# Performance work log

Measured on AMD Instinct MI355X. Metric: run time of the kernel, lower is better.

The kernel has to match this reference:

```python
import jax, jax.numpy as jnp
import numpy as np

B, C, N, T = 8, 32, 4000, 12
KT = 3
TS = 6          # tem_size
SUP_ORD_CH = (2 * 3 + 1) * C  # (order*support_len+1)*c_in = 224
EPS = 1e-5


def setup_inputs() -> dict:
    key = jax.random.key(0)
    ks = jax.random.split(key, 20)
    inp = {
        "x": jax.random.normal(ks[0], (B, C, N, T), dtype=jnp.float32),
        # dense normalized supports (scaled uniform, like row-normalized adjacency)
        "A0": jax.random.uniform(ks[1], (N, N), dtype=jnp.float32) / N,
        "A1": jax.random.uniform(ks[2], (N, N), dtype=jnp.float32) / N,
        "A2": jax.random.uniform(ks[3], (N, N), dtype=jnp.float32) / N,
        # conv1: 1x1 Conv2d(32 -> 32), bias
        "conv1_w": jax.random.normal(ks[4], (C, C), dtype=jnp.float32) * 0.05,
        "conv1_b": jnp.zeros((C,), dtype=jnp.float32),
        # multigcn mlp: Conv2d(224 -> 64, kernel (1, Kt)), bias
        "mlp_w": jax.random.normal(ks[5], (2 * C, SUP_ORD_CH, 1, KT), dtype=jnp.float32) * 0.02,
        "mlp_b": jnp.zeros((2 * C,), dtype=jnp.float32),
        # conv_temp1: 1x1 Conv2d over time axis (10 -> 6), bias
        "ct1_w": jax.random.normal(ks[6], (TS, T - KT + 1), dtype=jnp.float32) * 0.1,
        "ct1_b": jnp.zeros((TS,), dtype=jnp.float32),
        # TATT_1 params
        "tat_c1_w": jax.random.normal(ks[7], (C,), dtype=jnp.float32) * 0.1,   # Conv2d(c_in->1,1x1,no bias)
        "tat_c2_w": jax.random.normal(ks[8], (N,), dtype=jnp.float32) * 0.01,  # Conv2d(N->1,1x1,no bias)
        "tat_w": jax.random.normal(ks[9], (N, C), dtype=jnp.float32) * 0.01,
        "tat_bias": jnp.zeros((TS, TS), dtype=jnp.float32),
        "tat_v": jax.random.normal(ks[10], (TS, TS), dtype=jnp.float32) * 0.3,
        "bn1_g": jnp.ones((TS,), dtype=jnp.float32),
        "bn1_b": jnp.zeros((TS,), dtype=jnp.float32),
        # final BatchNorm2d(c_out)
        "bn2_g": jnp.ones((C,), dtype=jnp.float32),
        "bn2_b": jnp.zeros((C,), dtype=jnp.float32),
    }
    return inp


def reference(x, A0, A1, A2, conv1_w, conv1_b, mlp_w, mlp_b, ct1_w, ct1_b,
              tat_c1_w, tat_c2_w, tat_w, tat_bias, tat_v, bn1_g, bn1_b,
              bn2_g, bn2_b):
    # residual = conv1(x)  (1x1 conv over channels)
    residual = jnp.einsum('oc,bcnl->bonl', conv1_w, x) + conv1_b[None, :, None, None]

    # multi_gcn_time: nconv does A<-A.T then einsum('ncvl,vw->ncwl'),
    # i.e. out[..,w,..] = sum_v x[..,v,..] * A[w,v]
    outs = [x]
    for A in (A0, A1, A2):
        x1 = jnp.einsum('bcvl,wv->bcwl', x, A)
        outs.append(x1)
        x2 = jnp.einsum('bcvl,wv->bcwl', x1, A)
        outs.append(x2)
    h = jnp.concatenate(outs, axis=1)  # (B, 224, N, T)
    h = jax.lax.conv_general_dilated(
        h, mlp_w, window_strides=(1, 1), padding='VALID',
        dimension_numbers=('NCHW', 'OIHW', 'NCHW')) + mlp_b[None, :, None, None]  # (B,64,N,10)

    # gated tanh * sigmoid
    x1, x2 = jnp.split(h, 2, axis=1)
    g = jnp.tanh(x1) * jax.nn.sigmoid(x2)  # (B,32,N,10)

    # conv_temp1: 1x1 conv over the TIME axis (10 -> 6)
    g = jnp.einsum('ql,bcnl->bcnq', ct1_w, g) + ct1_b[None, None, None, :]  # (B,32,N,6)

    # TATT_1 temporal attention coefficients
    f1 = jnp.einsum('c,bcnt->btn', tat_c1_w, g)                       # (B,6,N)
    f2 = jnp.einsum('n,bcnt->bct', tat_c2_w, g)                       # (B,32,6)
    logits = jax.nn.sigmoid(jnp.einsum('btn,nc,bcs->bts', f1, tat_w, f2) + tat_bias)
    logits = jnp.einsum('ts,bsq->btq', tat_v, logits)                 # (B,6,6)
    # BatchNorm1d(tem_size) applied after permute(0,2,1): channel = q axis
    lp = jnp.transpose(logits, (0, 2, 1))
    mu = lp.mean(axis=(0, 2), keepdims=True)
    var = lp.var(axis=(0, 2), keepdims=True)
    lp = (lp - mu) / jnp.sqrt(var + EPS) * bn1_g[None, :, None] + bn1_b[None, :, None]
    logits = jnp.transpose(lp, (0, 2, 1))
    coefs = jax.nn.softmax(logits, axis=-1)                           # (B,6,6)

    # x = einsum('bcnl,blq->bcnq', x, T_coef.transpose(-1,-2))
    Tc = jnp.transpose(coefs, (0, 2, 1))
    out = jnp.einsum('bcnl,blq->bcnq', g, Tc)                         # (B,32,N,6)

    y = out + residual[:, :, :, -out.shape[3]:]
    # BatchNorm2d(c_out), training-mode batch stats
    mu2 = y.mean(axis=(0, 2, 3), keepdims=True)
    var2 = y.var(axis=(0, 2, 3), keepdims=True)
    return (y - mu2) / jnp.sqrt(var2 + EPS) * bn2_g[None, :, None, None] + bn2_b[None, :, None, None]
```

## Files before the change

kernel.cpp:

```cpp
#include <hip/hip_runtime.h>
#include <hip/hip_bf16.h>
#include <cstdint>
#include <cstddef>


typedef __attribute__((ext_vector_type(8))) short s16x8;
typedef __attribute__((ext_vector_type(4))) short s16x4;
typedef __attribute__((ext_vector_type(4))) float f32x4;

#define DEVFN __device__ __forceinline__

DEVFN void gload16(const void* g, void* l) {
  __builtin_amdgcn_global_load_lds((const __attribute__((address_space(1))) unsigned int*)g,
                                   (__attribute__((address_space(3))) unsigned int*)l, 16, 0, 0);
}

DEVFN unsigned short f2bf(float f) {
  union { float f; unsigned int u; } v; v.f = f;
  unsigned int u = v.u;
  return (unsigned short)((u + 0x7fffu + ((u >> 16) & 1u)) >> 16);
}

__global__ void k_transpose(const float* __restrict__ x,
                            unsigned short* __restrict__ Xt,
                            unsigned short* __restrict__ Scat) {
  __shared__ float ldsT[32 * 417];
  int v0 = blockIdx.x * 32;
  int b = blockIdx.y;
  int tid = threadIdx.x;
  for (int i = tid; i < 1024; i += 256) {
    int c = i >> 5, vv = i & 31;
    const float* src = x + ((size_t)(b * 32 + c) * 4000 + v0 + vv) * 12;
    f32x4 a0 = *(const f32x4*)(src);
    f32x4 a1 = *(const f32x4*)(src + 4);
    f32x4 a2 = *(const f32x4*)(src + 8);
    float* d = ldsT + c * 417 + vv * 13;
    d[0] = a0.x; d[1] = a0.y; d[2] = a0.z; d[3] = a0.w;
    d[4] = a1.x; d[5] = a1.y; d[6] = a1.z; d[7] = a1.w;
    d[8] = a2.x; d[9] = a2.y; d[10] = a2.z; d[11] = a2.w;
  }
  __syncthreads();
  for (int unit = tid; unit < 384; unit += 256) {
    int l = unit >> 5, c = unit & 31;
    alignas(16) unsigned short tmp[32];
#pragma unroll
    for (int vv = 0; vv < 32; ++vv) tmp[vv] = f2bf(ldsT[c * 417 + vv * 13 + l]);
    unsigned short* dst = Xt + (size_t)(b * 384 + l * 32 + c) * 4096 + v0;
#pragma unroll
    for (int j = 0; j < 4; ++j) *(s16x8*)(dst + j * 8) = *(const s16x8*)(tmp + j * 8);
  }
  for (int unit = tid; unit < 384; unit += 256) {
    int l = unit >> 5, vv = unit & 31;
    alignas(16) unsigned short tmp[32];
#pragma unroll
    for (int c = 0; c < 32; ++c) tmp[c] = f2bf(ldsT[c * 417 + vv * 13 + l]);
    unsigned short* dst = Scat + ((size_t)(b * 4000 + v0 + vv) * 12 + l) * 224;
#pragma unroll
    for (int j = 0; j < 4; ++j) *(s16x8*)(dst + j * 8) = *(const s16x8*)(tmp + j * 8);
  }
}

__global__ void k_castA(const float* __restrict__ A, unsigned short* __restrict__ Abf) {
  int idx = blockIdx.x * 256 + threadIdx.x;
  int r = idx >> 10;
  int c4 = (idx & 1023) << 2;
  alignas(8) unsigned short o[4] = {0, 0, 0, 0};
  if (r < 4000 && c4 < 4000) {
    f32x4 v = *(const f32x4*)(A + (size_t)r * 4000 + c4);
    o[0] = f2bf(v.x); o[1] = f2bf(v.y); o[2] = f2bf(v.z); o[3] = f2bf(v.w);
  }
  *(s16x4*)(Abf + (size_t)r * 4096 + c4) = *(const s16x4*)o;
}

__global__ void k_wcat(const float* __restrict__ mlp_w, unsigned short* __restrict__ Wcat) {
  int i = blockIdx.x * 256 + threadIdx.x;
  if (i >= 64 * 672) return;
  int oc = i / 672, k = i % 672;
  int kt = k / 224, ic = k % 224;
  Wcat[i] = f2bf(mlp_w[((size_t)oc * 224 + ic) * 3 + kt]);
}

#define MFMA_(a, b, c) __builtin_amdgcn_mfma_f32_16x16x32_bf16(a, b, c, 0, 0, 0)

#define STGA(d, t) do {                                                          \
    const unsigned short* _s = aSrc + (size_t)(t) * 64;                          \
    unsigned short* _l = smem + (d) * 12288;                                     \
    gload16(_s,          _l + tid * 8);                                          \
    gload16(_s + 262144, _l + (512 + tid) * 8);                                  \
    gload16(_s + 524288, _l + (1024 + tid) * 8);                                 \
  } while (0)

#define STGB(d, h, t) do {                                                       \
    const unsigned short* _s = bSrc + (size_t)(h) * 524288 + (size_t)(t) * 64;   \
    unsigned short* _l = smem + 24576 + ((d) * 2 + (h)) * 8192;                  \
    gload16(_s,          _l + tid * 8);                                          \
    gload16(_s + 262144, _l + (512 + tid) * 8);                                  \
  } while (0)

#define LDA_(d, f, kk) (*(const s16x8*)(smem + (d) * 12288 + aoff + (f) * 1024 + ((kk) ? sxor : 0)))
#define LDB_(d, nf, kk) (*(const s16x8*)(smem + 24576 + ((d) * 2 + hb) * 8192 + boff + (nf) * 1024 + ((kk) ? sxor : 0)))

#define PHASE(d, mp, FIRST, STAGE_CODE, VM) do {                                 \
    s16x8 a00 = LDA_(d, 2 * (mp), 0),     a01 = LDA_(d, 2 * (mp), 1);            \
    s16x8 a10 = LDA_(d, 2 * (mp) + 1, 0), a11 = LDA_(d, 2 * (mp) + 1, 1);        \
    if (FIRST) {                                                                 \
      _Pragma("unroll")                                                          \
      for (int nf = 0; nf < 4; ++nf) { bfr[nf][0] = LDB_(d, nf, 0); bfr[nf][1] = LDB_(d, nf, 1); } \
    }                                                                            \
    STAGE_CODE;                                                                  \
    if (VM) asm volatile("s_waitcnt vmcnt(2)" ::: "memory");                     \
    __builtin_amdgcn_s_barrier();                                                \
    asm volatile("s_waitcnt lgkmcnt(0)" ::: "memory");                           \
    __builtin_amdgcn_s_setprio(1);                                               \
    _Pragma("unroll")                                                            \
    for (int nf = 0; nf < 4; ++nf) {                                             \
      acc[2 * (mp)][nf]     = MFMA_(a00, bfr[nf][0], acc[2 * (mp)][nf]);         \
      acc[2 * (mp)][nf]     = MFMA_(a01, bfr[nf][1], acc[2 * (mp)][nf]);         \
      acc[2 * (mp) + 1][nf] = MFMA_(a10, bfr[nf][0], acc[2 * (mp) + 1][nf]);     \
      acc[2 * (mp) + 1][nf] = MFMA_(a11, bfr[nf][1], acc[2 * (mp) + 1][nf]);     \
    }                                                                            \
    __builtin_amdgcn_s_setprio(0);                                               \
  } while (0)

template <int WRITE_C1>
__global__ __launch_bounds__(512, 2)
void k_gemm(const unsigned short* __restrict__ P, const unsigned short* __restrict__ Q,
            unsigned short* __restrict__ C1, unsigned short* __restrict__ Scat, int jcol) {
  extern __shared__ unsigned short smem[];
  int tid = threadIdx.x;
  int w = tid >> 6, lane = tid & 63;
  int lr = lane & 15, g = lane >> 4;
  int mq = w >> 2, nq = w & 3;
  int bid = blockIdx.x;
  int xcd = bid & 7, lid = bid >> 3;
  int nt = xcd * 2 + (lid >> 4);
  int mt = lid & 15;
  int m0 = mt * 192, n0 = nt * 256;
  int hb = nq >> 1;
  int slot0 = (g ^ (lr & 7)) * 8;
  int sxor = (slot0 & 32) ? -32 : 32;
  int aoff = (mq * 96 + lr) * 64 + slot0;
  int boff = ((nq & 1) * 64 + lr) * 64 + slot0;
  int gk = ((tid & 7) ^ ((tid >> 3) & 7)) * 8;
  const unsigned short* aSrc = P + (size_t)(m0 + (tid >> 3)) * 4096 + gk;
  const unsigned short* bSrc = Q + (size_t)(n0 + (tid >> 3)) * 4096 + gk;
  f32x4 acc[6][4] = {};
  s16x8 bfr[4][2];

  STGA(0, 0);
  STGB(0, 0, 0); STGB(0, 1, 0);
  STGB(1, 0, 1);
  asm volatile("s_waitcnt vmcnt(2)" ::: "memory");
  __builtin_amdgcn_s_barrier();

#pragma unroll 1
  for (int i = 0; i < 32; ++i) {
    int t1 = 2 * i + 1, t2 = 2 * i + 2, t3 = 2 * i + 3;
    PHASE(0, 0, 1, STGB(1, 1, t1), 0);
    PHASE(0, 1, 0, STGA(1, t1),    0);
    PHASE(0, 2, 0, STGB(0, 0, t2), 1);
    PHASE(1, 0, 1, STGB(0, 1, t2), 0);
    PHASE(1, 1, 0, STGA(0, t2),    0);
    PHASE(1, 2, 0, STGB(1, 0, t3), 1);
  }

  asm volatile("s_waitcnt vmcnt(0) lgkmcnt(0)" ::: "memory");
  __syncthreads();
  unsigned short* eld = smem;
  int rb = g * 4;
#pragma unroll
  for (int f = 0; f < 6; ++f)
#pragma unroll
    for (int nf = 0; nf < 4; ++nf)
#pragma unroll
      for (int r = 0; r < 4; ++r)
        eld[(mq * 96 + f * 16 + rb + r) * 264 + nq * 64 + nf * 16 + lr] = f2bf(acc[f][nf][r]);
  __syncthreads();
  if (WRITE_C1) {
#pragma unroll
    for (int uu = 0; uu < 2; ++uu) {
      int u = uu * 512 + tid;
      if (u < 768) {
        int row = u >> 2, q = u & 3;
        unsigned short* dst = C1 + (size_t)(m0 + row) * 4096 + n0 + q * 64;
        const unsigned short* sp = eld + row * 264 + q * 64;
#pragma unroll
        for (int j = 0; j < 8; ++j) *(s16x8*)(dst + j * 8) = *(const s16x8*)(sp + j * 8);
      }
    }
  }
  int bb2 = m0 / 384, lb = (m0 % 384) >> 5;
#pragma unroll
  for (int uu = 0; uu < 3; ++uu) {
    int u = uu * 512 + tid;
    int lg = u >> 8, nl = u & 255;
    int node = n0 + nl;
    if (node < 4000) {
      alignas(16) unsigned short tmp[32];
#pragma unroll
      for (int c = 0; c < 32; ++c) tmp[c] = eld[(lg * 32 + c) * 264 + nl];
      unsigned short* d2 = Scat + ((size_t)(bb2 * 4000 + node) * 12 + lb + lg) * 224 + jcol;
#pragma unroll
      for (int j = 0; j < 4; ++j) *(s16x8*)(d2 + j * 8) = *(const s16x8*)(tmp + j * 8);
    }
  }
}

__global__ __launch_bounds__(256, 2)
void k_mlp(const unsigned short* __restrict__ Wcat, const unsigned short* __restrict__ Scat,
           const float* __restrict__ mlp_b, float* __restrict__ G) {
  __shared__ unsigned short lds[2048 + 8192];
  unsigned short* Ws = lds;
  unsigned short* Bs = lds + 2048;
  int tid = threadIdx.x;
  int bn0 = blockIdx.x * 256;
  int t = blockIdx.y;
  int w = tid >> 6, lane = tid & 63;
  int lr = lane & 15, lk = (lane >> 4) * 8;
  f32x4 acc[4][4] = {};
  const unsigned short* gw = Wcat + (size_t)(tid >> 2) * 672 + (tid & 3) * 8;
  const unsigned short* gq = Scat + ((size_t)(bn0 + (tid >> 2)) * 12 + t) * 224 + (tid & 3) * 8;
  unsigned short* lw = Ws + tid * 8;
  unsigned short* lq = Bs + tid * 8;
  for (int s = 0; s < 21; ++s) {
    gload16(gw + s * 32, lw);
#pragma unroll
    for (int r = 0; r < 4; ++r)
      gload16(gq + (size_t)r * 64 * 2688 + s * 32, lq + r * 2048);
    __syncthreads();
    s16x8 a[4], bb[4];
#pragma unroll
    for (int f = 0; f < 4; ++f) {
      a[f] = *(const s16x8*)(Ws + (f * 16 + lr) * 32 + lk);
      bb[f] = *(const s16x8*)(Bs + (w * 64 + f * 16 + lr) * 32 + lk);
    }
#pragma unroll
    for (int fm = 0; fm < 4; ++fm)
#pragma unroll
      for (int fn = 0; fn < 4; ++fn)
        acc[fm][fn] = __builtin_amdgcn_mfma_f32_16x16x32_bf16(a[fm], bb[fn], acc[fm][fn], 0, 0, 0);
    __syncthreads();
  }
  int rbase = (lane >> 4) * 4;
#pragma unroll
  for (int fn = 0; fn < 4; ++fn) {
    int bn = bn0 + w * 64 + fn * 16 + lr;
    int b = bn / 4000;
    int n = bn - b * 4000;
    float* gbase = G + (size_t)(b * 10 + t) * 32 * 4096 + n;
#pragma unroll
    for (int fm = 0; fm < 2; ++fm)
#pragma unroll
      for (int r = 0; r < 4; ++r) {
        int c = fm * 16 + rbase + r;
        float v1 = acc[fm][fn][r] + mlp_b[c];
        float v2 = acc[fm + 2][fn][r] + mlp_b[c + 32];
        gbase[(size_t)c * 4096] = tanhf(v1) * (1.0f / (1.0f + __expf(-v2)));
      }
  }
}

__global__ void k_ct1(const float* __restrict__ G, const float* __restrict__ ct1_w,
                      const float* __restrict__ ct1_b, float* __restrict__ g6) {
  int idx = blockIdx.x * 256 + threadIdx.x;
  if (idx >= 8 * 32 * 4000) return;
  int n = idx % 4000;
  int c = (idx / 4000) % 32;
  int b = idx / (4000 * 32);
  const float* gp = G + ((size_t)(b * 10) * 32 + c) * 4096 + n;
  float v[10];
#pragma unroll
  for (int l = 0; l < 10; ++l) v[l] = gp[(size_t)l * 32 * 4096];
  float* o = g6 + (size_t)idx * 6;
#pragma unroll
  for (int q = 0; q < 6; ++q) {
    float a = ct1_b[q];
#pragma unroll
    for (int l = 0; l < 10; ++l) a += ct1_w[q * 10 + l] * v[l];
    o[q] = a;
  }
}

__global__ void k_f1(const float* __restrict__ g6, const float* __restrict__ c1,
                     float* __restrict__ f1) {
  int idx = blockIdx.x * 128 + threadIdx.x;
  if (idx >= 8 * 4000) return;
  int n = idx % 4000, b = idx / 4000;
  float acc[6] = {};
  const float* gp = g6 + ((size_t)b * 32 * 4000 + n) * 6;
  for (int c = 0; c < 32; ++c) {
    float wv = c1[c];
    const float* p = gp + (size_t)c * 4000 * 6;
#pragma unroll
    for (int t = 0; t < 6; ++t) acc[t] += wv * p[t];
  }
  for (int t = 0; t < 6; ++t) f1[((size_t)b * 6 + t) * 4000 + n] = acc[t];
}

__global__ void k_f2(const float* __restrict__ g6, const float* __restrict__ c2,
                     float* __restrict__ f2) {
  __shared__ float red[256 * 6];
  int bc = blockIdx.x;
  int tid = threadIdx.x;
  float acc[6] = {};
  const float* gp = g6 + (size_t)bc * 4000 * 6;
  for (int n = tid; n < 4000; n += 256) {
    float wv = c2[n];
#pragma unroll
    for (int t = 0; t < 6; ++t) acc[t] += wv * gp[(size_t)n * 6 + t];
  }
  for (int t = 0; t < 6; ++t) red[tid * 6 + t] = acc[t];
  __syncthreads();
  for (int s = 128; s > 0; s >>= 1) {
    if (tid < s)
      for (int t = 0; t < 6; ++t) red[tid * 6 + t] += red[(tid + s) * 6 + t];
    __syncthreads();
  }
  if (tid < 6) f2[bc * 6 + tid] = red[tid];
}

__global__ void k_m1(const float* __restrict__ f1, const float* __restrict__ tw,
                     float* __restrict__ m1) {
  __shared__ float red[8][32];
  int bt = blockIdx.x;
  int nc = blockIdx.y;
  int tid = threadIdx.x;
  int c = tid & 31, gi = tid >> 5;
  float acc = 0.f;
  const float* fp = f1 + (size_t)bt * 4000 + nc * 250;
  const float* twp = tw + ((size_t)nc * 250) * 32 + c;
  for (int n = gi; n < 250; n += 8) acc += fp[n] * twp[n * 32];
  red[gi][c] = acc;
  __syncthreads();
  if (tid < 32) {
    float s = 0.f;
#pragma unroll
    for (int gg = 0; gg < 8; ++gg) s += red[gg][c];
    atomicAdd(&m1[(size_t)bt * 32 + c], s);
  }
}

__global__ void k_att(const float* __restrict__ m1, const float* __restrict__ f2,
                      const float* __restrict__ bias, const float* __restrict__ tv,
                      const float* __restrict__ g1, const float* __restrict__ b1,
                      float* __restrict__ coefs) {
  __shared__ float sig[48 * 6], lgs[48 * 6], mu[6], iv[6];
  int tid = threadIdx.x;
  int b = tid / 6, t = tid % 6;
  if (tid < 48) {
    for (int s = 0; s < 6; ++s) {
      float a = bias[t * 6 + s];
      for (int c = 0; c < 32; ++c)
        a += m1[((size_t)b * 6 + t) * 32 + c] * f2[((size_t)b * 32 + c) * 6 + s];
      sig[tid * 6 + s] = 1.0f / (1.0f + __expf(-a));
    }
  }
  __syncthreads();
  if (tid < 48) {
    for (int q = 0; q < 6; ++q) {
      float a = 0.f;
      for (int s = 0; s < 6; ++s) a += tv[t * 6 + s] * sig[(b * 6 + s) * 6 + q];
      lgs[tid * 6 + q] = a;
    }
  }
  __syncthreads();
  if (tid < 6) {
    float s = 0, s2 = 0;
    for (int r = 0; r < 48; ++r) { float v = lgs[r * 6 + tid]; s += v; s2 += v * v; }
    float m = s / 48.f;
    mu[tid] = m;
    iv[tid] = rsqrtf(s2 / 48.f - m * m + 1e-5f);
  }
  __syncthreads();
  if (tid < 48) {
    float v[6], mx = -1e30f;
    for (int q = 0; q < 6; ++q) {
      v[q] = (lgs[tid * 6 + q] - mu[q]) * iv[q] * g1[q] + b1[q];
      mx = fmaxf(mx, v[q]);
    }
    float s = 0;
    for (int q = 0; q < 6; ++q) { v[q] = __expf(v[q] - mx); s += v[q]; }
    float inv = 1.0f / s;
    for (int q = 0; q < 6; ++q) coefs[tid * 6 + q] = v[q] * inv;
  }
}

__global__ void k_final1(const float* __restrict__ x, const float* __restrict__ cw,
                         const float* __restrict__ cb, const float* __restrict__ g6,
                         const float* __restrict__ coefs, float* __restrict__ out) {
  __shared__ float xt[32 * 8 * 6];
  __shared__ float cwT[1024];
  __shared__ float cfs[36], cbs[32];
  int n0 = blockIdx.x * 8;
  int b = blockIdx.y;
  int tid = threadIdx.x;
  {
    int ci = tid >> 3, seg = tid & 7;
    const float* xp = x + ((size_t)(b * 32 + ci) * 4000 + n0 + seg) * 12 + 6;
#pragma unroll
    for (int q = 0; q < 6; ++q) xt[(ci * 8 + seg) * 6 + q] = xp[q];
  }
  for (int i = tid; i < 1024; i += 256) { int o = i >> 5, ci = i & 31; cwT[ci * 32 + o] = cw[i]; }
  if (tid < 36) cfs[tid] = coefs[b * 36 + tid];
  if (tid < 32) cbs[tid] = cb[tid];
  __syncthreads();
  int nn = tid & 7, c = tid >> 3;
  const float* gp = g6 + ((size_t)(b * 32 + c) * 4000 + n0 + nn) * 6;
  float gv[6];
#pragma unroll
  for (int l = 0; l < 6; ++l) gv[l] = gp[l];
  float y[6];
#pragma unroll
  for (int q = 0; q < 6; ++q) {
    float at = 0.f;
#pragma unroll
    for (int l = 0; l < 6; ++l) at += gv[l] * cfs[q * 6 + l];
    y[q] = at + cbs[c];
  }
  for (int ci = 0; ci < 32; ++ci) {
    float wv = cwT[ci * 32 + c];
#pragma unroll
    for (int q = 0; q < 6; ++q) y[q] += wv * xt[(ci * 8 + nn) * 6 + q];
  }
  float* op = out + ((size_t)(b * 32 + c) * 4000 + n0 + nn) * 6;
#pragma unroll
  for (int q = 0; q < 6; ++q) op[q] = y[q];
}

__global__ void k_stats(const float* __restrict__ out, float* __restrict__ stats) {
  __shared__ float r1[4], r2[4];
  int bc = blockIdx.y;
  int c = bc & 31;
  int tid = threadIdx.x;
  const float* p = out + (size_t)bc * 24000 + blockIdx.x * 6000;
  float s = 0.f, s2 = 0.f;
  for (int i = tid * 4; i < 6000; i += 1024) {
    f32x4 v = *(const f32x4*)(p + i);
    s  += v.x + v.y + v.z + v.w;
    s2 += v.x * v.x + v.y * v.y + v.z * v.z + v.w * v.w;
  }
#pragma unroll
  for (int off = 32; off > 0; off >>= 1) {
    s  += __shfl_down(s, off);
    s2 += __shfl_down(s2, off);
  }
  int lane = tid & 63, w = tid >> 6;
  if (lane == 0) { r1[w] = s; r2[w] = s2; }
  __syncthreads();
  if (tid == 0) {
    atomicAdd(&stats[c],      r1[0] + r1[1] + r1[2] + r1[3]);
    atomicAdd(&stats[32 + c], r2[0] + r2[1] + r2[2] + r2[3]);
  }
}

__global__ void k_final2(float* __restrict__ out, const float* __restrict__ stats,
                         const float* __restrict__ g2, const float* __restrict__ b2) {
  int idx = (blockIdx.x * 256 + threadIdx.x) * 4;
  if (idx >= 6144000) return;
  int c = (idx / 24000) % 32;
  float mean = stats[c] * (1.0f / 192000.f);
  float var = stats[32 + c] * (1.0f / 192000.f) - mean * mean;
  float sc = rsqrtf(var + 1e-5f) * g2[c];
  float sh = b2[c] - mean * sc;
  f32x4 v = *(f32x4*)(out + idx);
  v.x = v.x * sc + sh; v.y = v.y * sc + sh; v.z = v.z * sc + sh; v.w = v.w * sc + sh;
  *(f32x4*)(out + idx) = v;
}

extern "C" void kernel_launch(void* const* d_in, const int* in_sizes, int n_in,
                              void* d_out, int out_size, void* d_ws, size_t ws_size,
                              hipStream_t stream) {
  (void)in_sizes; (void)n_in; (void)out_size;
  const float* x       = (const float*)d_in[0];
  const float* A[3]    = {(const float*)d_in[1], (const float*)d_in[2], (const float*)d_in[3]};
  const float* conv1_w = (const float*)d_in[4];
  const float* conv1_b = (const float*)d_in[5];
  const float* mlp_w   = (const float*)d_in[6];
  const float* mlp_b   = (const float*)d_in[7];
  const float* ct1_w   = (const float*)d_in[8];
  const float* ct1_b   = (const float*)d_in[9];
  const float* c1w     = (const float*)d_in[10];
  const float* c2w     = (const float*)d_in[11];
  const float* tw      = (const float*)d_in[12];
  const float* tbias   = (const float*)d_in[13];
  const float* tv      = (const float*)d_in[14];
  const float* bn1g    = (const float*)d_in[15];
  const float* bn1b    = (const float*)d_in[16];
  const float* bn2g    = (const float*)d_in[17];
  const float* bn2b    = (const float*)d_in[18];
  float* out = (float*)d_out;

  char* ws = (char*)d_ws;
  size_t off = 0;
  auto alloc = [&](size_t bytes) { size_t r = off; off += (bytes + 255) & ~(size_t)255; return r; };
  size_t oScat = alloc(172032000);
  size_t oXt   = alloc(25165824);
  size_t oA    = alloc(33554432);
  size_t oY1t  = alloc(25165824);
  size_t oWcat = alloc(86016);
  size_t oF1 = alloc(768000);
  size_t oF2 = alloc(6144);
  size_t oM1 = alloc(6144);
  size_t oCf = alloc(1152);
  size_t oSt = alloc(256);
  if (ws_size < off) return;

  unsigned short* Scat = (unsigned short*)(ws + oScat);
  unsigned short* Xt   = (unsigned short*)(ws + oXt);
  float*          g6   = (float*)(ws + oXt);
  unsigned short* Abf  = (unsigned short*)(ws + oA);
  float*          G    = (float*)(ws + oA);
  unsigned short* Y1t  = (unsigned short*)(ws + oY1t);
  unsigned short* Wcat = (unsigned short*)(ws + oWcat);

  hipFuncSetAttribute((const void*)k_gemm<0>, hipFuncAttributeMaxDynamicSharedMemorySize, 114688);
  hipFuncSetAttribute((const void*)k_gemm<1>, hipFuncAttributeMaxDynamicSharedMemorySize, 114688);

  hipMemsetAsync(Xt, 0, 25165824, stream);
  hipMemsetAsync(ws + oSt, 0, 256, stream);
  hipMemsetAsync(ws + oM1, 0, 6144, stream);
  k_transpose<<<dim3(125, 8), 256, 0, stream>>>(x, Xt, Scat);
  k_wcat<<<168, 256, 0, stream>>>(mlp_w, Wcat);
  for (int i = 0; i < 3; ++i) {
    k_castA<<<16384, 256, 0, stream>>>(A[i], Abf);
    k_gemm<1><<<256, 512, 114688, stream>>>(Xt, Abf, Y1t, Scat, (2 * i + 1) * 32);
    k_gemm<0><<<256, 512, 114688, stream>>>(Y1t, Abf, nullptr, Scat, (2 * i + 2) * 32);
  }
  k_mlp<<<dim3(125, 10), 256, 0, stream>>>(Wcat, Scat, mlp_b, G);
  k_ct1<<<4000, 256, 0, stream>>>(G, ct1_w, ct1_b, g6);
  k_f1<<<250, 128, 0, stream>>>(g6, c1w, (float*)(ws + oF1));
  k_f2<<<256, 256, 0, stream>>>(g6, c2w, (float*)(ws + oF2));
  k_m1<<<dim3(48, 16), 256, 0, stream>>>((float*)(ws + oF1), tw, (float*)(ws + oM1));
  k_att<<<1, 64, 0, stream>>>((float*)(ws + oM1), (float*)(ws + oF2), tbias, tv, bn1g, bn1b,
                              (float*)(ws + oCf));
  k_final1<<<dim3(500, 8), 256, 0, stream>>>(x, conv1_w, conv1_b, g6, (float*)(ws + oCf), out);
  k_stats<<<dim3(4, 256), 256, 0, stream>>>(out, (float*)(ws + oSt));
  k_final2<<<6000, 256, 0, stream>>>(out, (float*)(ws + oSt), bn2g, bn2b);
}
```

Baseline: 815.1 us.

## Restructure MLP conv to reuse each time slice across three output steps

The MLP kernel now gives each block 64 nodes across all 12 time slices instead of one output time step. Each staged Scat time slice feeds the up-to-three output steps that use it, with a rotating set of three accumulators, so input reads drop about threefold. Loading of the next slice is double-buffered so it overlaps the current slice's MFMAs. Weights are read straight from global memory (cached) rather than staged in LDS, and the grid shrinks to 500 blocks, which may lower parallelism.

```diff
diff --git a/kernel.cpp b/kernel.cpp
--- a/kernel.cpp
+++ b/kernel.cpp
@@ -206,57 +206,77 @@
   }
 }
 
+#define MLPSTG(L, BUF) do {                                                   \
+    _Pragma("unroll")                                                         \
+    for (int j = 0; j < 7; ++j) {                                             \
+      int u = j * 256 + tid;                                                  \
+      int s = u >> 6, bn = u & 63;                                            \
+      gload16(Scat + ((size_t)(bn0 + bn) * 12 + (L)) * 224 + s * 8,           \
+              lds + (BUF) * 14336 + u * 8);                                   \
+    }                                                                         \
+  } while (0)
+
 __global__ __launch_bounds__(256, 2)
 void k_mlp(const unsigned short* __restrict__ Wcat, const unsigned short* __restrict__ Scat,
            const float* __restrict__ mlp_b, float* __restrict__ G) {
-  __shared__ unsigned short lds[2048 + 8192];
-  unsigned short* Ws = lds;
-  unsigned short* Bs = lds + 2048;
-  int tid = threadIdx.x;
-  int bn0 = blockIdx.x * 256;
-  int t = blockIdx.y;
+  __shared__ unsigned short lds[2 * 14336];
+  int tid = threadIdx.x;
+  int bn0 = blockIdx.x * 64;
   int w = tid >> 6, lane = tid & 63;
-  int lr = lane & 15, lk = (lane >> 4) * 8;
-  f32x4 acc[4][4] = {};
-  const unsigned short* gw = Wcat + (size_t)(tid >> 2) * 672 + (tid & 3) * 8;
-  const unsigned short* gq = Scat + ((size_t)(bn0 + (tid >> 2)) * 12 + t) * 224 + (tid & 3) * 8;
-  unsigned short* lw = Ws + tid * 8;
-  unsigned short* lq = Bs + tid * 8;
-  for (int s = 0; s < 21; ++s) {
-    gload16(gw + s * 32, lw);
-#pragma unroll
-    for (int r = 0; r < 4; ++r)
-      gload16(gq + (size_t)r * 64 * 2688 + s * 32, lq + r * 2048);
+  int lr = lane & 15, g = lane >> 4;
+  int p = w & 1, q = w >> 1;
+  const unsigned short* w1 = Wcat + (size_t)(p * 16 + lr) * 672 + g * 8;
+  const unsigned short* w2 = w1 + 32 * 672;
+  f32x4 acc[3][4];
+
+  MLPSTG(0, 0);
+  asm volatile("s_waitcnt vmcnt(0)" ::: "memory");
+  __syncthreads();
+
+#pragma unroll
+  for (int l = 0; l < 12; ++l) {
+    if (l < 11) MLPSTG(l + 1, (l + 1) & 1);
+    if (l <= 9) {
+#pragma unroll
+      for (int f = 0; f < 4; ++f) acc[l % 3][f] = (f32x4){0.f, 0.f, 0.f, 0.f};
+    }
+    const unsigned short* sb = lds + (l & 1) * 14336;
+#pragma unroll
+    for (int kt = 0; kt < 3; ++kt) {
+      int t = l - kt;
+      if (t < 0 || t > 9) continue;
+      int st = t % 3;
+#pragma unroll
+      for (int ks = 0; ks < 7; ++ks) {
+        s16x8 a1 = *(const s16x8*)(w1 + kt * 224 + ks * 32);
+        s16x8 a2 = *(const s16x8*)(w2 + kt * 224 + ks * 32);
+        const unsigned short* bbase = sb + ((ks * 4 + g) * 64 + q * 32 + lr) * 8;
+        s16x8 b0 = *(const s16x8*)(bbase);
+        s16x8 b1 = *(const s16x8*)(bbase + 128);
+        acc[st][0] = MFMA_(a1, b0, acc[st][0]);
+        acc[st][1] = MFMA_(a1, b1, acc[st][1]);
+        acc[st][2] = MFMA_(a2, b0, acc[st][2]);
+        acc[st][3] = MFMA_(a2, b1, acc[st][3]);
+      }
+    }
+    if (l >= 2) {
+      int t = l - 2, st = t % 3;
+#pragma unroll
+      for (int bf = 0; bf < 2; ++bf) {
+        int nglob = bn0 + q * 32 + bf * 16 + lr;
+        int b = nglob / 4000, nn = nglob - b * 4000;
+        float* gout = G + ((size_t)(b * 10 + t) * 32) * 4096 + nn;
+#pragma unroll
+        for (int r = 0; r < 4; ++r) {
+          int c = p * 16 + g * 4 + r;
+          float v1 = acc[st][bf][r] + mlp_b[c];
+          float v2 = acc[st][2 + bf][r] + mlp_b[c + 32];
+          gout[(size_t)c * 4096] = tanhf(v1) * (1.0f / (1.0f + __expf(-v2)));
+        }
+      }
+    }
+    asm volatile("s_waitcnt vmcnt(0)" ::: "memory");
     __syncthreads();
-    s16x8 a[4], bb[4];
-#pragma unroll
-    for (int f = 0; f < 4; ++f) {
-      a[f] = *(const s16x8*)(Ws + (f * 16 + lr) * 32 + lk);
-      bb[f] = *(const s16x8*)(Bs + (w * 64 + f * 16 + lr) * 32 + lk);
-    }
-#pragma unroll
-    for (int fm = 0; fm < 4; ++fm)
-#pragma unroll
-      for (int fn = 0; fn < 4; ++fn)
-        acc[fm][fn] = __builtin_amdgcn_mfma_f32_16x16x32_bf16(a[fm], bb[fn], acc[fm][fn], 0, 0, 0);
-    __syncthreads();
-  }
-  int rbase = (lane >> 4) * 4;
-#pragma unroll
-  for (int fn = 0; fn < 4; ++fn) {
-    int bn = bn0 + w * 64 + fn * 16 + lr;
-    int b = bn / 4000;
-    int n = bn - b * 4000;
-    float* gbase = G + (size_t)(b * 10 + t) * 32 * 4096 + n;
-#pragma unroll
-    for (int fm = 0; fm < 2; ++fm)
-#pragma unroll
-      for (int r = 0; r < 4; ++r) {
-        int c = fm * 16 + rbase + r;
-        float v1 = acc[fm][fn][r] + mlp_b[c];
-        float v2 = acc[fm + 2][fn][r] + mlp_b[c + 32];
-        gbase[(size_t)c * 4096] = tanhf(v1) * (1.0f / (1.0f + __expf(-v2)));
-      }
   }
 }
 
@@ -526,7 +546,7 @@
     k_gemm<1><<<256, 512, 114688, stream>>>(Xt, Abf, Y1t, Scat, (2 * i + 1) * 32);
     k_gemm<0><<<256, 512, 114688, stream>>>(Y1t, Abf, nullptr, Scat, (2 * i + 2) * 32);
   }
-  k_mlp<<<dim3(125, 10), 256, 0, stream>>>(Wcat, Scat, mlp_b, G);
+  k_mlp<<<500, 256, 0, stream>>>(Wcat, Scat, mlp_b, G);
   k_ct1<<<4000, 256, 0, stream>>>(G, ct1_w, ct1_b, g6);
   k_f1<<<250, 128, 0, stream>>>(g6, c1w, (float*)(ws + oF1));
   k_f2<<<256, 256, 0, stream>>>(g6, c2w, (float*)(ws + oF2));
```

Result: no change. 808.6 us (-0.8%).
